# Kernel optimization log

Hardware: AMD Instinct MI355X
Metric: run time of the kernel (lower is better)

## Reference

```python
import jax, jax.numpy as jnp
import numpy as np

B, S, F = 16, 511, 128           # batch, input seq len, n_features
D, H, NB = 512, 8, 6             # embedding_dim, n_heads, n_blocks
DH = D // H                      # d_head
MLP = 4 * D                      # mlp_ratio=4 hard-coded in FxtBlock
OUT = 1                          # out_d
T = S + 1                        # tokens incl. cls
EPS = 1e-5                       # torch LayerNorm default eps


def pos_emb(seq_len, d):
    # matches get_positional_embeddings: sin for even j, cos for odd j (with j-1 exponent)
    i = np.arange(seq_len, dtype=np.float32)[:, None]
    j = np.arange(d)
    je = np.where(j % 2 == 0, j, j - 1).astype(np.float32)
    ang = i / (10000.0 ** (je / d))
    pe = np.where(j % 2 == 0, np.sin(ang), np.cos(ang))
    return jnp.asarray(pe, jnp.float32)


def layernorm(x, g, b):
    m = jnp.mean(x, axis=-1, keepdims=True)
    v = jnp.mean((x - m) ** 2, axis=-1, keepdims=True)
    return (x - m) * jax.lax.rsqrt(v + EPS) * g + b


def setup_inputs() -> dict:
    key = jax.random.key(0)
    ks = jax.random.split(key, 12)
    g = lambda k, shape: jax.random.normal(k, shape, jnp.float32) * 0.02
    return {
        "src": jax.random.normal(ks[0], (B, S, F), jnp.float32),
        "emb_W": g(ks[1], (F, D)), "emb_b": jnp.zeros((D,), jnp.float32),
        "cls_tok": jax.random.uniform(ks[2], (1, D), jnp.float32),
        "ln1_g": jnp.ones((NB, D), jnp.float32), "ln1_b": jnp.zeros((NB, D), jnp.float32),
        "Wq": g(ks[3], (NB, H, DH, DH)), "bq": jnp.zeros((NB, H, DH), jnp.float32),
        "Wk": g(ks[4], (NB, H, DH, DH)), "bk": jnp.zeros((NB, H, DH), jnp.float32),
        "Wv": g(ks[5], (NB, H, DH, DH)), "bv": jnp.zeros((NB, H, DH), jnp.float32),
        "ln2_g": jnp.ones((NB, D), jnp.float32), "ln2_b": jnp.zeros((NB, D), jnp.float32),
        "W1": g(ks[6], (NB, D, MLP)), "b1": jnp.zeros((NB, MLP), jnp.float32),
        "W2": g(ks[7], (NB, MLP, D)), "b2": jnp.zeros((NB, D), jnp.float32),
        "head_W": g(ks[8], (D, OUT)), "head_b": jnp.zeros((OUT,), jnp.float32),
    }


def reference(src, emb_W, emb_b, cls_tok, ln1_g, ln1_b, Wq, bq, Wk, bk, Wv, bv,
              ln2_g, ln2_b, W1, b1, W2, b2, head_W, head_b):
    b = src.shape[0]
    x = src @ emb_W + emb_b                                    # [B,S,D]
    cls = jnp.broadcast_to(cls_tok[None], (b, 1, D))
    x = jnp.concatenate([cls, x], axis=1) + pos_emb(T, D)[None]  # [B,T,D]
    scale = 1.0 / jnp.sqrt(jnp.float32(DH))
    for i in range(NB):
        h = layernorm(x, ln1_g[i], ln1_b[i])
        hh = h.reshape(b, T, H, DH)
        q = jnp.einsum('bthd,hde->bhte', hh, Wq[i]) + bq[i][None, :, None, :]
        k = jnp.einsum('bthd,hde->bhte', hh, Wk[i]) + bk[i][None, :, None, :]
        v = jnp.einsum('bthd,hde->bhte', hh, Wv[i]) + bv[i][None, :, None, :]
        attn = jax.nn.softmax(jnp.einsum('bhse,bhte->bhst', q, k) * scale, axis=-1)
        o = jnp.einsum('bhst,bhte->bhse', attn, v)             # [B,H,T,DH]
        x = x + o.transpose(0, 2, 1, 3).reshape(b, T, D)
        h2 = layernorm(x, ln2_g[i], ln2_b[i])
        x = x + (jax.nn.gelu(h2 @ W1[i] + b1[i], approximate=False) @ W2[i] + b2[i])
    return jax.nn.sigmoid(x[:, 0] @ head_W + head_b)           # [B,OUT]
```

## Files before the change

kernel.cpp:

```cpp
#include <hip/hip_runtime.h>
#include <hip/hip_bf16.h>
#include <math.h>

#define B 16
#define S 511
#define F 128
#define D 512
#define H 8
#define NB 6
#define DH 64
#define MLPD 2048
#define T 512
#define EPS 1e-5f

typedef unsigned short ushort;
typedef __attribute__((ext_vector_type(8))) short short8;
typedef __attribute__((ext_vector_type(4))) float floatx4;

__device__ __forceinline__ ushort f2bf(float f) {
    union { float f; unsigned u; } cv; cv.f = f;
    unsigned r = (cv.u + 0x7fff + ((cv.u >> 16) & 1)) >> 16;
    return (ushort)r;
}

__device__ __forceinline__ float fast_gelu(float x) {
    float z = fabsf(x) * 0.70710678118f;
    float t = 1.0f / (1.0f + 0.3275911f * z);
    float p = ((((1.061405429f * t - 1.453152027f) * t + 1.421413741f) * t
               - 0.284496736f) * t + 0.254829592f) * t;
    float erfv = 1.0f - p * __expf(-z * z);
    erfv = copysignf(erfv, x);
    return 0.5f * x * (1.0f + erfv);
}

__global__ void castsrc_kernel(const float* __restrict__ src, ushort* __restrict__ srcb) {
    int row = blockIdx.x;
    int t = row & (T - 1), b = row >> 9;
    int tid = threadIdx.x;
    ushort v = 0;
    if (t > 0) v = f2bf(src[((size_t)b * S + (t - 1)) * F + tid]);
    srcb[(size_t)row * F + tid] = v;
}

__global__ void wtrans_kernel(const float* __restrict__ W,
                              ushort* __restrict__ Wt,
                              int K, int N) {
    int kb = blockIdx.x * 32, nb = blockIdx.y * 32, mat = blockIdx.z;
    __shared__ float tile[32][33];
    int tid = threadIdx.x;
    int c = tid & 31, r0 = tid >> 5;
    const float* Wm = W + (size_t)mat * K * N;
    ushort* Wtm = Wt + (size_t)mat * K * N;
    #pragma unroll
    for (int l = 0; l < 4; ++l) {
        int r = r0 + l * 8;
        tile[r][c] = Wm[(size_t)(kb + r) * N + nb + c];
    }
    __syncthreads();
    #pragma unroll
    for (int l = 0; l < 4; ++l) {
        int r = r0 + l * 8;
        Wtm[(size_t)(nb + r) * K + kb + c] = f2bf(tile[c][r]);
    }
}

__global__ void wtransq_kernel(const float* __restrict__ Wq, const float* __restrict__ Wk,
                               const float* __restrict__ Wv,
                               ushort* __restrict__ WqT, ushort* __restrict__ WkT,
                               ushort* __restrict__ WvT) {
    int mat = blockIdx.x;
    int which = blockIdx.y;
    const float* W = (which == 0 ? Wq : which == 1 ? Wk : Wv) + (size_t)mat * 4096;
    ushort* O = (which == 0 ? WqT : which == 1 ? WkT : WvT) + (size_t)mat * 4096;
    __shared__ float t[64][65];
    int tid = threadIdx.x;
    int r0 = tid >> 6, c = tid & 63;
    #pragma unroll
    for (int l = 0; l < 16; ++l) {
        int row = r0 * 16 + l;
        t[row][c] = W[row * 64 + c];
    }
    __syncthreads();
    #pragma unroll
    for (int l = 0; l < 16; ++l) {
        int row = r0 * 16 + l;
        O[row * 64 + c] = f2bf(t[c][row]);
    }
}

__device__ __forceinline__ void gload_lds16(const ushort* g, ushort* l) {
    __builtin_amdgcn_global_load_lds((const __attribute__((address_space(1))) unsigned int*)g,
                                     (__attribute__((address_space(3))) unsigned int*)l,
                                     16, 0, 0);
}

#define S_WAITCNT_VM(N) asm volatile("s_waitcnt vmcnt(" #N ")" ::: "memory")

__global__ __launch_bounds__(256) void embed_gemm(const ushort* __restrict__ A,
                                                  const ushort* __restrict__ Bt,
                                                  const float* __restrict__ emb_b,
                                                  const float* __restrict__ cls_tok,
                                                  float* __restrict__ x) {
    __shared__ ushort As[64 * 32];
    __shared__ ushort Bs[64 * 32];
    int tid = threadIdx.x;
    int lane = tid & 63;
    int w = __builtin_amdgcn_readfirstlane(tid >> 6);
    int quad = lane >> 4, l15 = lane & 15;
    int wr = (w >> 1) * 32, wc = (w & 1) * 32;
    int m0 = blockIdx.x * 64, n0 = blockIdx.y * 64;

    floatx4 acc[2][2];
    #pragma unroll
    for (int i = 0; i < 2; ++i)
        #pragma unroll
        for (int j = 0; j < 2; ++j) acc[i][j] = (floatx4)0.f;

    int lrow = lane >> 2;
    int lk = (lane & 3) * 8;
    const ushort* Ag = A + (size_t)(m0 + 16 * w + lrow) * F + lk;
    const ushort* Bg = Bt + (size_t)(n0 + 16 * w + lrow) * F + lk;
    ushort* AsW = &As[16 * w * 32];
    ushort* BsW = &Bs[16 * w * 32];
    int fa = l15 * 32 + quad * 8;

    for (int kt = 0; kt < F; kt += 32) {
        gload_lds16(Ag + kt, AsW);
        gload_lds16(Bg + kt, BsW);
        __syncthreads();
        short8 af[2], bf[2];
        #pragma unroll
        for (int i = 0; i < 2; ++i) af[i] = *(const short8*)&As[(wr + 16 * i) * 32 + fa];
        #pragma unroll
        for (int j = 0; j < 2; ++j) bf[j] = *(const short8*)&Bs[(wc + 16 * j) * 32 + fa];
        #pragma unroll
        for (int i = 0; i < 2; ++i)
            #pragma unroll
            for (int j = 0; j < 2; ++j)
                acc[i][j] = __builtin_amdgcn_mfma_f32_16x16x32_bf16(af[i], bf[j], acc[i][j], 0, 0, 0);
        __syncthreads();
    }

    const float LOG1E4 = 9.210340371976184f;
    int rbase = (lane >> 4) * 4;
    int cidx = lane & 15;
    #pragma unroll
    for (int j = 0; j < 2; ++j) {
        int gc = n0 + wc + 16 * j + cidx;
        float je = (float)(gc & ~1);
        float freq = expf(-(je / (float)D) * LOG1E4);
        float ebv = emb_b[gc];
        float clsv = cls_tok[gc];
        bool odd = (gc & 1);
        #pragma unroll
        for (int i = 0; i < 2; ++i) {
            int gr = m0 + wr + 16 * i + rbase;
            #pragma unroll
            for (int reg = 0; reg < 4; ++reg) {
                int row = gr + reg;
                int t = row & (T - 1);
                float ang = (float)t * freq;
                float pe = odd ? cosf(ang) : sinf(ang);
                float val = (t == 0) ? (clsv + pe) : (acc[i][j][reg] + ebv + pe);
                x[(size_t)row * D + gc] = val;
            }
        }
    }
}

__global__ __launch_bounds__(256) void ln_kernel(const float* __restrict__ xin,
                                                 const float* __restrict__ g,
                                                 const float* __restrict__ bb,
                                                 ushort* __restrict__ out) {
    int lane = threadIdx.x & 63;
    int row = blockIdx.x * 4 + (threadIdx.x >> 6);
    const float* xr = xin + (size_t)row * D + lane * 8;
    float4 a0 = *(const float4*)xr;
    float4 a1 = *(const float4*)(xr + 4);
    float s = a0.x + a0.y + a0.z + a0.w + a1.x + a1.y + a1.z + a1.w;
    #pragma unroll
    for (int off = 1; off < 64; off <<= 1) s += __shfl_xor(s, off);
    float mean = s * (1.0f / (float)D);
    float d0 = a0.x - mean, d1 = a0.y - mean, d2 = a0.z - mean, d3 = a0.w - mean;
    float d4 = a1.x - mean, d5 = a1.y - mean, d6 = a1.z - mean, d7 = a1.w - mean;
    float sq = d0*d0 + d1*d1 + d2*d2 + d3*d3 + d4*d4 + d5*d5 + d6*d6 + d7*d7;
    #pragma unroll
    for (int off = 1; off < 64; off <<= 1) sq += __shfl_xor(sq, off);
    float rstd = rsqrtf(sq * (1.0f / (float)D) + EPS);
    const float* gp = g + lane * 8;
    const float* bp = bb + lane * 8;
    float4 g0 = *(const float4*)gp, g1 = *(const float4*)(gp + 4);
    float4 b0 = *(const float4*)bp, b1 = *(const float4*)(bp + 4);
    short8 o;
    o[0] = (short)f2bf(d0 * rstd * g0.x + b0.x);
    o[1] = (short)f2bf(d1 * rstd * g0.y + b0.y);
    o[2] = (short)f2bf(d2 * rstd * g0.z + b0.z);
    o[3] = (short)f2bf(d3 * rstd * g0.w + b0.w);
    o[4] = (short)f2bf(d4 * rstd * g1.x + b1.x);
    o[5] = (short)f2bf(d5 * rstd * g1.y + b1.y);
    o[6] = (short)f2bf(d6 * rstd * g1.z + b1.z);
    o[7] = (short)f2bf(d7 * rstd * g1.w + b1.w);
    *(short8*)(out + (size_t)row * D + lane * 8) = o;
}

__global__ __launch_bounds__(256) void ln_fuse_kernel(float* __restrict__ x,
                                                      const float* __restrict__ p0,
                                                      const float* __restrict__ g,
                                                      const float* __restrict__ bb,
                                                      ushort* __restrict__ out) {
    int lane = threadIdx.x & 63;
    int row = blockIdx.x * 4 + (threadIdx.x >> 6);
    size_t base = (size_t)row * D + lane * 8;
    float* xr = x + base;
    float4 a0 = *(const float4*)xr;
    float4 a1 = *(const float4*)(xr + 4);
    float4 q0 = *(const float4*)(p0 + base);
    float4 q1 = *(const float4*)(p0 + base + 4);
    a0.x += q0.x; a0.y += q0.y; a0.z += q0.z; a0.w += q0.w;
    a1.x += q1.x; a1.y += q1.y; a1.z += q1.z; a1.w += q1.w;
    *(float4*)xr = a0;
    *(float4*)(xr + 4) = a1;
    float s = a0.x + a0.y + a0.z + a0.w + a1.x + a1.y + a1.z + a1.w;
    #pragma unroll
    for (int off = 1; off < 64; off <<= 1) s += __shfl_xor(s, off);
    float mean = s * (1.0f / (float)D);
    float d0 = a0.x - mean, d1 = a0.y - mean, d2 = a0.z - mean, d3 = a0.w - mean;
    float d4 = a1.x - mean, d5 = a1.y - mean, d6 = a1.z - mean, d7 = a1.w - mean;
    float sq = d0*d0 + d1*d1 + d2*d2 + d3*d3 + d4*d4 + d5*d5 + d6*d6 + d7*d7;
    #pragma unroll
    for (int off = 1; off < 64; off <<= 1) sq += __shfl_xor(sq, off);
    float rstd = rsqrtf(sq * (1.0f / (float)D) + EPS);
    const float* gp = g + lane * 8;
    const float* bp = bb + lane * 8;
    float4 g0 = *(const float4*)gp, g1 = *(const float4*)(gp + 4);
    float4 b0 = *(const float4*)bp, b1 = *(const float4*)(bp + 4);
    short8 o;
    o[0] = (short)f2bf(d0 * rstd * g0.x + b0.x);
    o[1] = (short)f2bf(d1 * rstd * g0.y + b0.y);
    o[2] = (short)f2bf(d2 * rstd * g0.z + b0.z);
    o[3] = (short)f2bf(d3 * rstd * g0.w + b0.w);
    o[4] = (short)f2bf(d4 * rstd * g1.x + b1.x);
    o[5] = (short)f2bf(d5 * rstd * g1.y + b1.y);
    o[6] = (short)f2bf(d6 * rstd * g1.z + b1.z);
    o[7] = (short)f2bf(d7 * rstd * g1.w + b1.w);
    *(short8*)(out + (size_t)row * D + lane * 8) = o;
}

__global__ __launch_bounds__(256) void qkv_kernel(
        const ushort* __restrict__ hb,
        const ushort* __restrict__ WqT, const float* __restrict__ bq,
        const ushort* __restrict__ WkT, const float* __restrict__ bk,
        const ushort* __restrict__ WvT, const float* __restrict__ bv,
        ushort* __restrict__ qo, ushort* __restrict__ ko, ushort* __restrict__ vTo) {
    int m0 = blockIdx.x * 128;
    int hh = blockIdx.y;
    int tid = threadIdx.x;
    int lane = tid & 63;
    int w = __builtin_amdgcn_readfirstlane(tid >> 6);
    int quad = lane >> 4, l15 = lane & 15;

    short8 af[2][2];
    #pragma unroll
    for (int mt = 0; mt < 2; ++mt) {
        const ushort* ab = hb + (size_t)(m0 + w * 32 + mt * 16 + l15) * D + hh * DH + quad * 8;
        af[mt][0] = *(const short8*)(ab);
        af[mt][1] = *(const short8*)(ab + 32);
    }

    floatx4 acc[3][2][4];
    #pragma unroll
    for (int xo = 0; xo < 3; ++xo)
        #pragma unroll
        for (int mt = 0; mt < 2; ++mt)
            #pragma unroll
            for (int nt = 0; nt < 4; ++nt) acc[xo][mt][nt] = (floatx4)0.f;

    #pragma unroll
    for (int xo = 0; xo < 3; ++xo) {
        const ushort* WT = (xo == 0 ? WqT : xo == 1 ? WkT : WvT) + (size_t)hh * 4096;
        #pragma unroll
        for (int nt = 0; nt < 4; ++nt) {
            const ushort* wb = WT + (size_t)(nt * 16 + l15) * 64 + quad * 8;
            short8 bf0 = *(const short8*)(wb);
            short8 bf1 = *(const short8*)(wb + 32);
            #pragma unroll
            for (int mt = 0; mt < 2; ++mt) {
                acc[xo][mt][nt] = __builtin_amdgcn_mfma_f32_16x16x32_bf16(af[mt][0], bf0, acc[xo][mt][nt], 0, 0, 0);
                acc[xo][mt][nt] = __builtin_amdgcn_mfma_f32_16x16x32_bf16(af[mt][1], bf1, acc[xo][mt][nt], 0, 0, 0);
            }
        }
    }

    int bb = m0 >> 9;
    int bh = bb * H + hh;
    #pragma unroll
    for (int mt = 0; mt < 2; ++mt) {
        int trow = m0 + w * 32 + mt * 16 + quad * 4;
        int tt = trow & (T - 1);
        #pragma unroll
        for (int nt = 0; nt < 4; ++nt) {
            int col = nt * 16 + l15;
            float bqv = bq[hh * DH + col];
            float bkv = bk[hh * DH + col];
            float bvv = bv[hh * DH + col];
            #pragma unroll
            for (int reg = 0; reg < 4; ++reg) {
                qo[((size_t)bh * T + tt + reg) * DH + col] = f2bf(acc[0][mt][nt][reg] + bqv);
                ko[((size_t)bh * T + tt + reg) * DH + col] = f2bf(acc[1][mt][nt][reg] + bkv);
                vTo[((size_t)bh * DH + col) * T + tt + reg] = f2bf(acc[2][mt][nt][reg] + bvv);
            }
        }
    }
}

#define PSTRIDE 88
__global__ __launch_bounds__(256) void attn_kernel(const ushort* __restrict__ q,
                                                   const ushort* __restrict__ k,
                                                   const ushort* __restrict__ vT,
                                                   float* __restrict__ x) {
    int bh = blockIdx.x;
    int qt = blockIdx.y;
    int b = bh >> 3, hh = bh & 7;
    int tid = threadIdx.x;
    int lane = tid & 63;
    int w = __builtin_amdgcn_readfirstlane(tid >> 6);
    int quad = lane >> 4, l15 = lane & 15;

    __shared__ __align__(16) ushort smem[22016];
    ushort* Pw = smem + 16384 + w * (16 * PSTRIDE);

    const ushort* qbase = q + ((size_t)bh * T + qt * 64 + w * 16 + l15) * DH + quad * 8;
    short8 Qf0 = *(const short8*)(qbase);
    short8 Qf1 = *(const short8*)(qbase + 32);

    const ushort* kbase = k + (size_t)bh * T * DH;
    const ushort* vbase = vT + (size_t)bh * DH * T;

    int srow = lane >> 2;
    int scol = (lane & 3) * 8;
    const ushort* kg = kbase + (size_t)(w * 16 + srow) * DH + scol;
    const ushort* vg = vbase + (size_t)(w * 16 + srow) * T + scol;
    ushort* ldsK = smem + w * 16 * 32;
    ushort* ldsV = smem + 8192 + w * 16 * 32;

    float l_i[4] = {0.f, 0.f, 0.f, 0.f};
    floatx4 O[4];
    #pragma unroll
    for (int j = 0; j < 4; ++j) O[j] = (floatx4)0.f;

    gload_lds16(kg, ldsK);
    gload_lds16(kg + 32, ldsK + 2048);
    gload_lds16(vg, ldsV);
    gload_lds16(vg + 32, ldsV + 2048);
    __syncthreads();

    for (int kt = 0; kt < T / 64; ++kt) {
        int cur = kt & 1;
        if (kt < T / 64 - 1) {
            int nb = cur ^ 1;
            const ushort* kgn = kg + (size_t)(kt + 1) * 64 * DH;
            const ushort* vgn = vg + (kt + 1) * 64;
            gload_lds16(kgn, ldsK + nb * 4096);
            gload_lds16(kgn + 32, ldsK + nb * 4096 + 2048);
            gload_lds16(vgn, ldsV + nb * 4096);
            gload_lds16(vgn + 32, ldsV + nb * 4096 + 2048);
        }
        const ushort* Kc = smem + cur * 4096;
        const ushort* Vc = smem + 8192 + cur * 4096;

        floatx4 sc[4];
        #pragma unroll
        for (int j = 0; j < 4; ++j) {
            int ro = (j * 16 + l15) * 32 + quad * 8;
            short8 kf0 = *(const short8*)&Kc[ro];
            short8 kf1 = *(const short8*)&Kc[2048 + ro];
            floatx4 s4 = (floatx4)0.f;
            s4 = __builtin_amdgcn_mfma_f32_16x16x32_bf16(Qf0, kf0, s4, 0, 0, 0);
            s4 = __builtin_amdgcn_mfma_f32_16x16x32_bf16(Qf1, kf1, s4, 0, 0, 0);
            sc[j] = s4;
        }
        #pragma unroll
        for (int j = 0; j < 4; ++j) {
            #pragma unroll
            for (int r = 0; r < 4; ++r) {
                float p = __expf(sc[j][r] * 0.125f);
                ushort pb = f2bf(p);
                union { unsigned u; float f; } cv; cv.u = ((unsigned)pb) << 16;
                l_i[r] += cv.f;
                Pw[(quad * 4 + r) * PSTRIDE + j * 16 + l15] = pb;
            }
        }

        short8 af0 = *(const short8*)&Pw[l15 * PSTRIDE + quad * 8];
        short8 af1 = *(const short8*)&Pw[l15 * PSTRIDE + 32 + quad * 8];
        #pragma unroll
        for (int j = 0; j < 4; ++j) {
            int ro = (j * 16 + l15) * 32 + quad * 8;
            short8 vf0 = *(const short8*)&Vc[ro];
            short8 vf1 = *(const short8*)&Vc[2048 + ro];
            O[j] = __builtin_amdgcn_mfma_f32_16x16x32_bf16(af0, vf0, O[j], 0, 0, 0);
            O[j] = __builtin_amdgcn_mfma_f32_16x16x32_bf16(af1, vf1, O[j], 0, 0, 0);
        }
        __syncthreads();
    }

    #pragma unroll
    for (int r = 0; r < 4; ++r) {
        l_i[r] += __shfl_xor(l_i[r], 1);
        l_i[r] += __shfl_xor(l_i[r], 2);
        l_i[r] += __shfl_xor(l_i[r], 4);
        l_i[r] += __shfl_xor(l_i[r], 8);
    }

    float* Ow = (float*)smem + w * 16 * 68;
    #pragma unroll
    for (int r = 0; r < 4; ++r) {
        float rl = 1.0f / l_i[r];
        #pragma unroll
        for (int j = 0; j < 4; ++j)
            Ow[(quad * 4 + r) * 68 + j * 16 + l15] = O[j][r] * rl;
    }
    __syncthreads();
    int r4 = lane >> 4;
    int c16 = lane & 15;
    #pragma unroll
    for (int i = 0; i < 4; ++i) {
        int lrow = i * 4 + r4;
        float4 o = *(const float4*)&Ow[lrow * 68 + c16 * 4];
        int grow = qt * 64 + w * 16 + lrow;
        float* xp = &x[((size_t)(b * T) + grow) * D + hh * DH + c16 * 4];
        float4 xv = *(const float4*)xp;
        xv.x += o.x; xv.y += o.y; xv.z += o.z; xv.w += o.w;
        *(float4*)xp = xv;
    }
}

template<int BM, int EPI>
__global__ __launch_bounds__(512) void gemm_pipe(const ushort* __restrict__ A,
                                                 const ushort* __restrict__ Bt,
                                                 const float* __restrict__ bias,
                                                 void* __restrict__ Cout,
                                                 int N, int K) {
    constexpr int BN = 128;
    constexpr int BK = 64;
    constexpr int MREP = BM / 32;
    constexpr int AJ = BM / 64;
    constexpr int TILE = (BM + BN) * BK;
    __shared__ ushort lds[3 * TILE];

    int tid = threadIdx.x;
    int lane = tid & 63;
    int w = __builtin_amdgcn_readfirstlane(tid >> 6);
    int quad = lane >> 4, l15 = lane & 15;
    int wrow = (w >> 2) * (BM / 2);
    int wcol = (w & 3) * 32;
    int m0 = blockIdx.x * BM, n0 = blockIdx.y * BN;

    int lrow8 = lane >> 3;
    int lslot = lane & 7;
    int scol = (lslot ^ lrow8) * 8;
    const ushort* Asrc = A + (size_t)(m0 + w * 8 + lrow8) * K + scol;
    const ushort* Bsrc = Bt + (size_t)(n0 + w * 8 + lrow8) * K + scol;
    ushort* ldsA0 = lds + (w * 8) * BK;
    ushort* ldsB0 = lds + BM * BK + (w * 8) * BK;

    int sx0 = ((quad) ^ (l15 & 7)) * 8;
    int sx1 = ((4 + quad) ^ (l15 & 7)) * 8;

    floatx4 acc[MREP][2];
    #pragma unroll
    for (int i = 0; i < MREP; ++i) {
        acc[i][0] = (floatx4)0.f;
        acc[i][1] = (floatx4)0.f;
    }

    #define STAGE_T(t, buf) do {                                                   \
        const ushort* ap_ = Asrc + (size_t)(t) * BK;                               \
        const ushort* bp_ = Bsrc + (size_t)(t) * BK;                               \
        ushort* la_ = ldsA0 + (buf) * TILE;                                        \
        ushort* lb_ = ldsB0 + (buf) * TILE;                                        \
        _Pragma("unroll")                                                          \
        for (int j = 0; j < AJ; ++j)                                               \
            gload_lds16(ap_ + (size_t)j * 64 * K, la_ + j * 64 * BK);              \
        _Pragma("unroll")                                                          \
        for (int j = 0; j < 2; ++j)                                                \
            gload_lds16(bp_ + (size_t)j * 64 * K, lb_ + j * 64 * BK);              \
    } while (0)

    #define COMPUTE_T(buf) do {                                                    \
        const ushort* Ab_ = lds + (buf) * TILE;                                    \
        const ushort* Bb_ = Ab_ + BM * BK;                                         \
        _Pragma("unroll")                                                          \
        for (int ks = 0; ks < 2; ++ks) {                                           \
            int sx_ = ks ? sx1 : sx0;                                              \
            short8 bfr0 = *(const short8*)&Bb_[(wcol + l15) * BK + sx_];           \
            short8 bfr1 = *(const short8*)&Bb_[(wcol + 16 + l15) * BK + sx_];      \
            _Pragma("unroll")                                                      \
            for (int i = 0; i < MREP; ++i) {                                       \
                short8 af_ = *(const short8*)&Ab_[(wrow + i * 16 + l15) * BK + sx_]; \
                acc[i][0] = __builtin_amdgcn_mfma_f32_16x16x32_bf16(af_, bfr0, acc[i][0], 0, 0, 0); \
                acc[i][1] = __builtin_amdgcn_mfma_f32_16x16x32_bf16(af_, bfr1, acc[i][1], 0, 0, 0); \
            }                                                                      \
        }                                                                          \
    } while (0)

    STAGE_T(0, 0);
    STAGE_T(1, 1);

    int NT = K / BK;
    int cb = 0, nbuf = 2;
    for (int t = 0; t < NT - 2; ++t) {
        STAGE_T(t + 2, nbuf);
        if constexpr (AJ == 4) { S_WAITCNT_VM(12); } else { S_WAITCNT_VM(8); }
        __builtin_amdgcn_s_barrier();
        __builtin_amdgcn_s_setprio(1);
        COMPUTE_T(cb);
        __builtin_amdgcn_s_setprio(0);
        asm volatile("s_waitcnt lgkmcnt(0)" ::: "memory");
        __builtin_amdgcn_s_barrier();
        cb = (cb == 2) ? 0 : cb + 1;
        nbuf = (nbuf == 2) ? 0 : nbuf + 1;
    }
    if constexpr (AJ == 4) { S_WAITCNT_VM(6); } else { S_WAITCNT_VM(4); }
    __builtin_amdgcn_s_barrier();
    __builtin_amdgcn_s_setprio(1);
    COMPUTE_T(cb);
    __builtin_amdgcn_s_setprio(0);
    asm volatile("s_waitcnt lgkmcnt(0)" ::: "memory");
    __builtin_amdgcn_s_barrier();
    cb = (cb == 2) ? 0 : cb + 1;
    S_WAITCNT_VM(0);
    __builtin_amdgcn_s_barrier();
    COMPUTE_T(cb);

    #undef STAGE_T
    #undef COMPUTE_T

    int rbase = quad * 4;
    #pragma unroll
    for (int i = 0; i < MREP; ++i) {
        #pragma unroll
        for (int n = 0; n < 2; ++n) {
            int gc = n0 + wcol + n * 16 + l15;
            float bv = bias[gc];
            int gr = m0 + wrow + i * 16 + rbase;
            #pragma unroll
            for (int reg = 0; reg < 4; ++reg) {
                if constexpr (EPI == 0) {
                    ((ushort*)Cout)[(size_t)(gr + reg) * N + gc] =
                        f2bf(fast_gelu(acc[i][n][reg] + bv));
                } else {
                    ((float*)Cout)[(size_t)(gr + reg) * N + gc] = acc[i][n][reg] + bv;
                }
            }
        }
    }
}

__global__ void head_kernel(const float* __restrict__ x,
                            const float* __restrict__ p0,
                            const float* __restrict__ hw,
                            const float* __restrict__ hb,
                            float* __restrict__ out) {
    int b = blockIdx.x;
    int tid = threadIdx.x;
    size_t idx = (size_t)b * T * D + tid;
    float s = (x[idx] + p0[idx]) * hw[tid];
    #pragma unroll
    for (int off = 32; off > 0; off >>= 1) s += __shfl_down(s, off, 64);
    __shared__ float red[8];
    if ((tid & 63) == 0) red[tid >> 6] = s;
    __syncthreads();
    if (tid == 0) {
        float t = 0.f;
        #pragma unroll
        for (int i = 0; i < 8; ++i) t += red[i];
        out[b] = 1.0f / (1.0f + __expf(-(t + hb[0])));
    }
}

extern "C" void kernel_launch(void* const* d_in, const int* in_sizes, int n_in,
                              void* d_out, int out_size, void* d_ws, size_t ws_size,
                              hipStream_t stream) {
    const float* src     = (const float*)d_in[0];
    const float* emb_W   = (const float*)d_in[1];
    const float* emb_b   = (const float*)d_in[2];
    const float* cls_tok = (const float*)d_in[3];
    const float* ln1_g   = (const float*)d_in[4];
    const float* ln1_b   = (const float*)d_in[5];
    const float* Wq      = (const float*)d_in[6];
    const float* bq      = (const float*)d_in[7];
    const float* Wk      = (const float*)d_in[8];
    const float* bk      = (const float*)d_in[9];
    const float* Wv      = (const float*)d_in[10];
    const float* bv      = (const float*)d_in[11];
    const float* ln2_g   = (const float*)d_in[12];
    const float* ln2_b   = (const float*)d_in[13];
    const float* W1      = (const float*)d_in[14];
    const float* b1      = (const float*)d_in[15];
    const float* W2      = (const float*)d_in[16];
    const float* b2      = (const float*)d_in[17];
    const float* head_W  = (const float*)d_in[18];
    const float* head_b  = (const float*)d_in[19];

    const size_t NTOK = (size_t)B * T;
    char* wsb = (char*)d_ws;
    float*  x    = (float*)wsb;      wsb += NTOK * D * 4;
    float*  p0   = (float*)wsb;      wsb += NTOK * D * 4;
    ushort* hbuf = (ushort*)wsb;     wsb += NTOK * D * 2;
    ushort* q    = (ushort*)wsb;     wsb += NTOK * D * 2;
    ushort* k    = (ushort*)wsb;     wsb += NTOK * D * 2;
    ushort* vT   = (ushort*)wsb;     wsb += NTOK * D * 2;
    ushort* u    = (ushort*)wsb;     wsb += NTOK * MLPD * 2;
    ushort* W1t  = (ushort*)wsb;     wsb += (size_t)NB * D * MLPD * 2;
    ushort* W2t  = (ushort*)wsb;     wsb += (size_t)NB * D * MLPD * 2;
    ushort* WqT  = (ushort*)wsb;     wsb += (size_t)NB * H * DH * DH * 2;
    ushort* WkT  = (ushort*)wsb;     wsb += (size_t)NB * H * DH * DH * 2;
    ushort* WvT  = (ushort*)wsb;     wsb += (size_t)NB * H * DH * DH * 2;
    ushort* srcb = (ushort*)wsb;     wsb += NTOK * F * 2;
    ushort* embWt= (ushort*)wsb;     wsb += (size_t)F * D * 2;

    wtrans_kernel<<<dim3(D / 32, MLPD / 32, NB), 256, 0, stream>>>(W1, W1t, D, MLPD);
    wtrans_kernel<<<dim3(MLPD / 32, D / 32, NB), 256, 0, stream>>>(W2, W2t, MLPD, D);
    wtransq_kernel<<<dim3(NB * H, 3), 256, 0, stream>>>(Wq, Wk, Wv, WqT, WkT, WvT);
    wtrans_kernel<<<dim3(F / 32, D / 32, 1), 256, 0, stream>>>(emb_W, embWt, F, D);
    castsrc_kernel<<<B * T, F, 0, stream>>>(src, srcb);

    embed_gemm<<<dim3(B * T / 64, D / 64), 256, 0, stream>>>(srcb, embWt, emb_b, cls_tok, x);

    for (int i = 0; i < NB; ++i) {
        if (i == 0)
            ln_kernel<<<B * T / 4, 256, 0, stream>>>(x, ln1_g, ln1_b, hbuf);
        else
            ln_fuse_kernel<<<B * T / 4, 256, 0, stream>>>(x, p0,
                ln1_g + i * D, ln1_b + i * D, hbuf);
        qkv_kernel<<<dim3(B * T / 128, H), 256, 0, stream>>>(hbuf,
            WqT + (size_t)i * H * DH * DH, bq + (size_t)i * H * DH,
            WkT + (size_t)i * H * DH * DH, bk + (size_t)i * H * DH,
            WvT + (size_t)i * H * DH * DH, bv + (size_t)i * H * DH,
            q, k, vT);
        attn_kernel<<<dim3(B * H, T / 64), 256, 0, stream>>>(q, k, vT, x);
        ln_kernel<<<B * T / 4, 256, 0, stream>>>(x, ln2_g + i * D, ln2_b + i * D, hbuf);
        gemm_pipe<256, 0><<<dim3(B * T / 256, MLPD / 128), 512, 0, stream>>>(
            hbuf, W1t + (size_t)i * D * MLPD, b1 + (size_t)i * MLPD, u, MLPD, D);
        gemm_pipe<128, 1><<<dim3(B * T / 128, D / 128), 512, 0, stream>>>(
            u, W2t + (size_t)i * MLPD * D, b2 + (size_t)i * D, p0, D, MLPD);
    }

    head_kernel<<<B, 512, 0, stream>>>(x, p0, head_W, head_b, (float*)d_out);
}
```

Baseline: 814.9 us.

## Replace MLP GEMMs with 128x128 double-buffered kernel and XCD-aware tile remap

Replaces the triple-buffered 512-thread MLP GEMM with a 256-thread kernel that computes 128x128 tiles, where each wave owns a 64x64 sub-tile (4x4 MFMA accumulators). Shared memory is cut to two buffers so two blocks can share a CU (launch_bounds 256,2). A 1D grid with a block-id remap groups neighbouring tiles onto the same XCD to improve L2 reuse. The aim is more operand reuse per LDS load and better occupancy, traded against a shallower prefetch pipeline and higher register pressure from 64 accumulators per thread.

```diff
diff --git a/kernel.cpp b/kernel.cpp
--- a/kernel.cpp
+++ b/kernel.cpp
@@ -435,112 +435,119 @@
     }
 }
 
-template<int BM, int EPI>
-__global__ __launch_bounds__(512) void gemm_pipe(const ushort* __restrict__ A,
-                                                 const ushort* __restrict__ Bt,
-                                                 const float* __restrict__ bias,
-                                                 void* __restrict__ Cout,
-                                                 int N, int K) {
-    constexpr int BN = 128;
+template<int EPI>
+__global__ __launch_bounds__(256, 2) void gemm_db(const ushort* __restrict__ A,
+                                                  const ushort* __restrict__ Bt,
+                                                  const float* __restrict__ bias,
+                                                  void* __restrict__ Cout,
+                                                  int N, int K) {
     constexpr int BK = 64;
-    constexpr int MREP = BM / 32;
-    constexpr int AJ = BM / 64;
-    constexpr int TILE = (BM + BN) * BK;
-    __shared__ ushort lds[3 * TILE];
+    __shared__ ushort lds0[256 * BK];
+    __shared__ ushort lds1[256 * BK];
 
     int tid = threadIdx.x;
     int lane = tid & 63;
     int w = __builtin_amdgcn_readfirstlane(tid >> 6);
     int quad = lane >> 4, l15 = lane & 15;
-    int wrow = (w >> 2) * (BM / 2);
-    int wcol = (w & 3) * 32;
-    int m0 = blockIdx.x * BM, n0 = blockIdx.y * BN;
-
-    int lrow8 = lane >> 3;
-    int lslot = lane & 7;
-    int scol = (lslot ^ lrow8) * 8;
-    const ushort* Asrc = A + (size_t)(m0 + w * 8 + lrow8) * K + scol;
-    const ushort* Bsrc = Bt + (size_t)(n0 + w * 8 + lrow8) * K + scol;
-    ushort* ldsA0 = lds + (w * 8) * BK;
-    ushort* ldsB0 = lds + BM * BK + (w * 8) * BK;
+    int wrow = (w >> 1) * 64;
+    int wcol = (w & 1) * 64;
+
+    int nwg = gridDim.x;
+    int id = blockIdx.x;
+    int idx = (id & 7) * (nwg >> 3) + (id >> 3);
+    int NTg = N >> 7;
+    int mt = idx / NTg;
+    int nt = idx - mt * NTg;
+    int m0 = mt * 128, n0 = nt * 128;
+
+    int lrow = tid >> 3;
+    int lslot = tid & 7;
+    int scol = (lslot ^ (lrow & 7)) * 8;
+    const ushort* Asrc = A + (size_t)(m0 + lrow) * K + scol;
+    const ushort* Bsrc = Bt + (size_t)(n0 + lrow) * K + scol;
+    int ldsAoff = (w * 8) * BK;
+    int ldsBoff = 128 * BK + (w * 8) * BK;
 
     int sx0 = ((quad) ^ (l15 & 7)) * 8;
     int sx1 = ((4 + quad) ^ (l15 & 7)) * 8;
 
-    floatx4 acc[MREP][2];
-    #pragma unroll
-    for (int i = 0; i < MREP; ++i) {
-        acc[i][0] = (floatx4)0.f;
-        acc[i][1] = (floatx4)0.f;
-    }
-
-    #define STAGE_T(t, buf) do {                                                   \
-        const ushort* ap_ = Asrc + (size_t)(t) * BK;                               \
-        const ushort* bp_ = Bsrc + (size_t)(t) * BK;                               \
-        ushort* la_ = ldsA0 + (buf) * TILE;                                        \
-        ushort* lb_ = ldsB0 + (buf) * TILE;                                        \
-        _Pragma("unroll")                                                          \
-        for (int j = 0; j < AJ; ++j)                                               \
-            gload_lds16(ap_ + (size_t)j * 64 * K, la_ + j * 64 * BK);              \
-        _Pragma("unroll")                                                          \
-        for (int j = 0; j < 2; ++j)                                                \
-            gload_lds16(bp_ + (size_t)j * 64 * K, lb_ + j * 64 * BK);              \
+    floatx4 acc[4][4];
+    #pragma unroll
+    for (int i = 0; i < 4; ++i)
+        #pragma unroll
+        for (int n = 0; n < 4; ++n) acc[i][n] = (floatx4)0.f;
+
+    #define STAGE(t, Lb) do {                                                     \
+        const ushort* ap_ = Asrc + (size_t)(t) * BK;                              \
+        const ushort* bp_ = Bsrc + (size_t)(t) * BK;                              \
+        _Pragma("unroll")                                                         \
+        for (int j = 0; j < 4; ++j)                                               \
+            gload_lds16(ap_ + (size_t)j * 32 * K, (Lb) + ldsAoff + j * 32 * BK);  \
+        _Pragma("unroll")                                                         \
+        for (int j = 0; j < 4; ++j)                                               \
+            gload_lds16(bp_ + (size_t)j * 32 * K, (Lb) + ldsBoff + j * 32 * BK);  \
     } while (0)
 
-    #define COMPUTE_T(buf) do {                                                    \
-        const ushort* Ab_ = lds + (buf) * TILE;                                    \
-        const ushort* Bb_ = Ab_ + BM * BK;                                         \
-        _Pragma("unroll")                                                          \
-        for (int ks = 0; ks < 2; ++ks) {                                           \
-            int sx_ = ks ? sx1 : sx0;                                              \
-            short8 bfr0 = *(const short8*)&Bb_[(wcol + l15) * BK + sx_];           \
-            short8 bfr1 = *(const short8*)&Bb_[(wcol + 16 + l15) * BK + sx_];      \
-            _Pragma("unroll")                                                      \
-            for (int i = 0; i < MREP; ++i) {                                       \
+    #define COMP(Lb) do {                                                         \
+        const ushort* Ab_ = (Lb);                                                 \
+        const ushort* Bb_ = (Lb) + 128 * BK;                                      \
+        _Pragma("unroll")                                                         \
+        for (int ks = 0; ks < 2; ++ks) {                                          \
+            int sx_ = ks ? sx1 : sx0;                                             \
+            short8 bfr[4];                                                        \
+            _Pragma("unroll")                                                     \
+            for (int n = 0; n < 4; ++n)                                           \
+                bfr[n] = *(const short8*)&Bb_[(wcol + n * 16 + l15) * BK + sx_];  \
+            _Pragma("unroll")                                                     \
+            for (int i = 0; i < 4; ++i) {                                         \
                 short8 af_ = *(const short8*)&Ab_[(wrow + i * 16 + l15) * BK + sx_]; \
-                acc[i][0] = __builtin_amdgcn_mfma_f32_16x16x32_bf16(af_, bfr0, acc[i][0], 0, 0, 0); \
-                acc[i][1] = __builtin_amdgcn_mfma_f32_16x16x32_bf16(af_, bfr1, acc[i][1], 0, 0, 0); \
-            }                                                                      \
-        }                                                                          \
+                _Pragma("unroll")                                                 \
+                for (int n = 0; n < 4; ++n)                                       \
+                    acc[i][n] = __builtin_amdgcn_mfma_f32_16x16x32_bf16(af_, bfr[n], acc[i][n], 0, 0, 0); \
+            }                                                                     \
+        }                                                                         \
     } while (0)
 
-    STAGE_T(0, 0);
-    STAGE_T(1, 1);
-
-    int NT = K / BK;
-    int cb = 0, nbuf = 2;
-    for (int t = 0; t < NT - 2; ++t) {
-        STAGE_T(t + 2, nbuf);
-        if constexpr (AJ == 4) { S_WAITCNT_VM(12); } else { S_WAITCNT_VM(8); }
+    int NT = K >> 6;
+    STAGE(0, lds0);
+    for (int t = 0; t < NT - 2; t += 2) {
+        STAGE(t + 1, lds1);
+        S_WAITCNT_VM(8);
         __builtin_amdgcn_s_barrier();
         __builtin_amdgcn_s_setprio(1);
-        COMPUTE_T(cb);
+        COMP(lds0);
         __builtin_amdgcn_s_setprio(0);
         asm volatile("s_waitcnt lgkmcnt(0)" ::: "memory");
         __builtin_amdgcn_s_barrier();
-        cb = (cb == 2) ? 0 : cb + 1;
-        nbuf = (nbuf == 2) ? 0 : nbuf + 1;
-    }
-    if constexpr (AJ == 4) { S_WAITCNT_VM(6); } else { S_WAITCNT_VM(4); }
+        STAGE(t + 2, lds0);
+        S_WAITCNT_VM(8);
+        __builtin_amdgcn_s_barrier();
+        __builtin_amdgcn_s_setprio(1);
+        COMP(lds1);
+        __builtin_amdgcn_s_setprio(0);
+        asm volatile("s_waitcnt lgkmcnt(0)" ::: "memory");
+        __builtin_amdgcn_s_barrier();
+    }
+    STAGE(NT - 1, lds1);
+    S_WAITCNT_VM(8);
     __builtin_amdgcn_s_barrier();
     __builtin_amdgcn_s_setprio(1);
-    COMPUTE_T(cb);
+    COMP(lds0);
     __builtin_amdgcn_s_setprio(0);
     asm volatile("s_waitcnt lgkmcnt(0)" ::: "memory");
     __builtin_amdgcn_s_barrier();
-    cb = (cb == 2) ? 0 : cb + 1;
     S_WAITCNT_VM(0);
     __builtin_amdgcn_s_barrier();
-    COMPUTE_T(cb);
-
-    #undef STAGE_T
-    #undef COMPUTE_T
+    COMP(lds1);
+
+    #undef STAGE
+    #undef COMP
 
     int rbase = quad * 4;
     #pragma unroll
-    for (int i = 0; i < MREP; ++i) {
-        #pragma unroll
-        for (int n = 0; n < 2; ++n) {
+    for (int i = 0; i < 4; ++i) {
+        #pragma unroll
+        for (int n = 0; n < 4; ++n) {
             int gc = n0 + wcol + n * 16 + l15;
             float bv = bias[gc];
             int gr = m0 + wrow + i * 16 + rbase;
@@ -641,9 +648,9 @@
             q, k, vT);
         attn_kernel<<<dim3(B * H, T / 64), 256, 0, stream>>>(q, k, vT, x);
         ln_kernel<<<B * T / 4, 256, 0, stream>>>(x, ln2_g + i * D, ln2_b + i * D, hbuf);
-        gemm_pipe<256, 0><<<dim3(B * T / 256, MLPD / 128), 512, 0, stream>>>(
+        gemm_db<0><<<dim3((B * T / 128) * (MLPD / 128)), 256, 0, stream>>>(
             hbuf, W1t + (size_t)i * D * MLPD, b1 + (size_t)i * MLPD, u, MLPD, D);
-        gemm_pipe<128, 1><<<dim3(B * T / 128, D / 128), 512, 0, stream>>>(
+        gemm_db<1><<<dim3((B * T / 128) * (D / 128)), 256, 0, stream>>>(
             u, W2t + (size_t)i * MLPD * D, b2 + (size_t)i * D, p0, D, MLPD);
     }
 
```

New measurement: 848.9 us. 4.2% more time.

## Compute only CLS token rows in final block and fuse MLP with head

Applied to the files above, without the earlier changes.

In the last block, attention runs only for the first query tile, and the full LN2+MLP GEMMs are replaced by a single-workgroup tail kernel. That kernel layer-norms the 16 CLS rows, runs both MLP matmuls with MFMA and applies the sigmoid head. This removes the last block's full-sequence MLP and most of its attention, since only the CLS token reaches the output. The softmax denominator now accumulates unrounded fp32 probabilities rather than bf16-rounded ones, a small numerical change. The single-workgroup tail streams all W1/W2 weights through one CU, which could be slow.

```diff
diff --git a/kernel.cpp b/kernel.cpp
--- a/kernel.cpp
+++ b/kernel.cpp
@@ -384,10 +384,8 @@
             #pragma unroll
             for (int r = 0; r < 4; ++r) {
                 float p = __expf(sc[j][r] * 0.125f);
-                ushort pb = f2bf(p);
-                union { unsigned u; float f; } cv; cv.u = ((unsigned)pb) << 16;
-                l_i[r] += cv.f;
-                Pw[(quad * 4 + r) * PSTRIDE + j * 16 + l15] = pb;
+                l_i[r] += p;
+                Pw[(quad * 4 + r) * PSTRIDE + j * 16 + l15] = f2bf(p);
             }
         }
 
@@ -557,26 +555,107 @@
     }
 }
 
-__global__ void head_kernel(const float* __restrict__ x,
-                            const float* __restrict__ p0,
-                            const float* __restrict__ hw,
-                            const float* __restrict__ hb,
-                            float* __restrict__ out) {
-    int b = blockIdx.x;
+#define HPAD 520
+#define UPAD 2056
+__global__ __launch_bounds__(512) void tail_kernel(
+        const float* __restrict__ x,
+        const float* __restrict__ g, const float* __restrict__ bb,
+        const ushort* __restrict__ W1t, const float* __restrict__ b1,
+        const ushort* __restrict__ W2t, const float* __restrict__ b2,
+        const float* __restrict__ hw, const float* __restrict__ hb,
+        float* __restrict__ out) {
+    __shared__ ushort h2s[16 * HPAD];
+    __shared__ ushort us[16 * UPAD];
+    __shared__ float mlps[16 * 512];
     int tid = threadIdx.x;
-    size_t idx = (size_t)b * T * D + tid;
-    float s = (x[idx] + p0[idx]) * hw[tid];
-    #pragma unroll
-    for (int off = 32; off > 0; off >>= 1) s += __shfl_down(s, off, 64);
-    __shared__ float red[8];
-    if ((tid & 63) == 0) red[tid >> 6] = s;
+    int lane = tid & 63;
+    int w = __builtin_amdgcn_readfirstlane(tid >> 6);
+    int quad = lane >> 4, l15 = lane & 15;
+
+    #pragma unroll
+    for (int p = 0; p < 2; ++p) {
+        int r = w * 2 + p;
+        const float* xr = x + (size_t)r * T * D + lane * 8;
+        float4 a0 = *(const float4*)xr;
+        float4 a1 = *(const float4*)(xr + 4);
+        float s = a0.x + a0.y + a0.z + a0.w + a1.x + a1.y + a1.z + a1.w;
+        #pragma unroll
+        for (int off = 1; off < 64; off <<= 1) s += __shfl_xor(s, off);
+        float mean = s * (1.0f / (float)D);
+        float d0 = a0.x - mean, d1 = a0.y - mean, d2 = a0.z - mean, d3 = a0.w - mean;
+        float d4 = a1.x - mean, d5 = a1.y - mean, d6 = a1.z - mean, d7 = a1.w - mean;
+        float sq = d0*d0 + d1*d1 + d2*d2 + d3*d3 + d4*d4 + d5*d5 + d6*d6 + d7*d7;
+        #pragma unroll
+        for (int off = 1; off < 64; off <<= 1) sq += __shfl_xor(sq, off);
+        float rstd = rsqrtf(sq * (1.0f / (float)D) + EPS);
+        const float* gp = g + lane * 8;
+        const float* bp = bb + lane * 8;
+        float4 g0 = *(const float4*)gp, g1 = *(const float4*)(gp + 4);
+        float4 b0 = *(const float4*)bp, b1v = *(const float4*)(bp + 4);
+        short8 o;
+        o[0] = (short)f2bf(d0 * rstd * g0.x + b0.x);
+        o[1] = (short)f2bf(d1 * rstd * g0.y + b0.y);
+        o[2] = (short)f2bf(d2 * rstd * g0.z + b0.z);
+        o[3] = (short)f2bf(d3 * rstd * g0.w + b0.w);
+        o[4] = (short)f2bf(d4 * rstd * g1.x + b1v.x);
+        o[5] = (short)f2bf(d5 * rstd * g1.y + b1v.y);
+        o[6] = (short)f2bf(d6 * rstd * g1.z + b1v.z);
+        o[7] = (short)f2bf(d7 * rstd * g1.w + b1v.w);
+        *(short8*)(h2s + r * HPAD + lane * 8) = o;
+    }
     __syncthreads();
-    if (tid == 0) {
-        float t = 0.f;
-        #pragma unroll
-        for (int i = 0; i < 8; ++i) t += red[i];
-        out[b] = 1.0f / (1.0f + __expf(-(t + hb[0])));
-    }
+
+    short8 af[16];
+    #pragma unroll
+    for (int ks = 0; ks < 16; ++ks)
+        af[ks] = *(const short8*)&h2s[l15 * HPAD + ks * 32 + quad * 8];
+    #pragma unroll
+    for (int nf = 0; nf < 16; ++nf) {
+        int nb = w * 256 + nf * 16;
+        const ushort* wrow = W1t + (size_t)(nb + l15) * D + quad * 8;
+        floatx4 acc = (floatx4)0.f;
+        #pragma unroll
+        for (int ks = 0; ks < 16; ++ks) {
+            short8 bf = *(const short8*)(wrow + ks * 32);
+            acc = __builtin_amdgcn_mfma_f32_16x16x32_bf16(af[ks], bf, acc, 0, 0, 0);
+        }
+        float bv = b1[nb + l15];
+        #pragma unroll
+        for (int reg = 0; reg < 4; ++reg)
+            us[(quad * 4 + reg) * UPAD + nb + l15] = f2bf(fast_gelu(acc[reg] + bv));
+    }
+    __syncthreads();
+
+    #pragma unroll
+    for (int nf = 0; nf < 4; ++nf) {
+        int nb = w * 64 + nf * 16;
+        const ushort* wrow = W2t + (size_t)(nb + l15) * MLPD + quad * 8;
+        floatx4 acc = (floatx4)0.f;
+        #pragma unroll 8
+        for (int ks = 0; ks < 64; ++ks) {
+            short8 a2 = *(const short8*)&us[l15 * UPAD + ks * 32 + quad * 8];
+            short8 bf = *(const short8*)(wrow + ks * 32);
+            acc = __builtin_amdgcn_mfma_f32_16x16x32_bf16(a2, bf, acc, 0, 0, 0);
+        }
+        float bv = b2[nb + l15];
+        #pragma unroll
+        for (int reg = 0; reg < 4; ++reg)
+            mlps[(quad * 4 + reg) * 512 + nb + l15] = acc[reg] + bv;
+    }
+    __syncthreads();
+
+    int r = w * 2 + (lane >> 5);
+    int l31 = lane & 31;
+    const float* xc = x + (size_t)r * T * D;
+    float s = 0.f;
+    #pragma unroll
+    for (int j = 0; j < 16; ++j) {
+        int c = l31 + j * 32;
+        s += (xc[c] + mlps[r * 512 + c]) * hw[c];
+    }
+    s += __shfl_xor(s, 16); s += __shfl_xor(s, 8); s += __shfl_xor(s, 4);
+    s += __shfl_xor(s, 2); s += __shfl_xor(s, 1);
+    if (l31 == 0) out[r] = 1.0f / (1.0f + __expf(-(s + hb[0])));
 }
 
 extern "C" void kernel_launch(void* const* d_in, const int* in_sizes, int n_in,
@@ -639,13 +718,20 @@
             WkT + (size_t)i * H * DH * DH, bk + (size_t)i * H * DH,
             WvT + (size_t)i * H * DH * DH, bv + (size_t)i * H * DH,
             q, k, vT);
-        attn_kernel<<<dim3(B * H, T / 64), 256, 0, stream>>>(q, k, vT, x);
-        ln_kernel<<<B * T / 4, 256, 0, stream>>>(x, ln2_g + i * D, ln2_b + i * D, hbuf);
-        gemm_pipe<256, 0><<<dim3(B * T / 256, MLPD / 128), 512, 0, stream>>>(
-            hbuf, W1t + (size_t)i * D * MLPD, b1 + (size_t)i * MLPD, u, MLPD, D);
-        gemm_pipe<128, 1><<<dim3(B * T / 128, D / 128), 512, 0, stream>>>(
-            u, W2t + (size_t)i * MLPD * D, b2 + (size_t)i * D, p0, D, MLPD);
-    }
-
-    head_kernel<<<B, 512, 0, stream>>>(x, p0, head_W, head_b, (float*)d_out);
-}
+        if (i < NB - 1) {
+            attn_kernel<<<dim3(B * H, T / 64), 256, 0, stream>>>(q, k, vT, x);
+            ln_kernel<<<B * T / 4, 256, 0, stream>>>(x, ln2_g + i * D, ln2_b + i * D, hbuf);
+            gemm_pipe<256, 0><<<dim3(B * T / 256, MLPD / 128), 512, 0, stream>>>(
+                hbuf, W1t + (size_t)i * D * MLPD, b1 + (size_t)i * MLPD, u, MLPD, D);
+            gemm_pipe<128, 1><<<dim3(B * T / 128, D / 128), 512, 0, stream>>>(
+                u, W2t + (size_t)i * MLPD * D, b2 + (size_t)i * D, p0, D, MLPD);
+        } else {
+            attn_kernel<<<dim3(B * H, 1), 256, 0, stream>>>(q, k, vT, x);
+            tail_kernel<<<1, 512, 0, stream>>>(x,
+                ln2_g + (size_t)i * D, ln2_b + (size_t)i * D,
+                W1t + (size_t)i * D * MLPD, b1 + (size_t)i * MLPD,
+                W2t + (size_t)i * MLPD * D, b2 + (size_t)i * D,
+                head_W, head_b, (float*)d_out);
+        }
+    }
+}
```

Result: slower. 874.6 us (+7.3%).
